# Kernel tuning notes

Measured on AMD Instinct MI355X. Metric: run time of the kernel, lower is better.

The kernel has to match this reference:

```python
import jax, jax.numpy as jnp
import numpy as np

OBS_DIM = 512
BACKBONE_DIMS = [1024, 1024, 512]
EXPERT_HIDDEN = 256
NUM_EXPERTS = 16
NUM_ACTIONS = 32
BATCH = 65536


def _glorot(key, shape):
    fan_in = shape[-2] if len(shape) >= 2 else shape[-1]
    return jax.random.normal(key, shape, dtype=jnp.float32) * (1.0 / np.sqrt(fan_in))


def setup_inputs() -> dict:
    key = jax.random.key(0)
    ks = jax.random.split(key, 16)
    inp = {}
    inp['obs'] = jax.random.normal(ks[0], (BATCH, OBS_DIM), dtype=jnp.float32)
    # shared backbone: 512->1024->1024->512 (Linear+ReLU+Dropout(eval=identity))
    dims = [OBS_DIM] + BACKBONE_DIMS
    for i in range(3):
        inp[f'Wb{i}'] = _glorot(ks[1 + i], (dims[i], dims[i + 1]))
        inp[f'bb{i}'] = jnp.zeros((dims[i + 1],), dtype=jnp.float32)
    # experts, batched over expert dim: 512->256->ReLU->256->32
    inp['We1'] = _glorot(ks[4], (NUM_EXPERTS, BACKBONE_DIMS[-1], EXPERT_HIDDEN))
    inp['be1'] = jnp.zeros((NUM_EXPERTS, EXPERT_HIDDEN), dtype=jnp.float32)
    inp['We2'] = _glorot(ks[5], (NUM_EXPERTS, EXPERT_HIDDEN, NUM_ACTIONS))
    inp['be2'] = jnp.zeros((NUM_EXPERTS, NUM_ACTIONS), dtype=jnp.float32)
    # motion selector: 512->256->128->16 + softmax
    inp['Ws0'] = _glorot(ks[6], (OBS_DIM, 256))
    inp['bs0'] = jnp.zeros((256,), dtype=jnp.float32)
    inp['Ws1'] = _glorot(ks[7], (256, 128))
    inp['bs1'] = jnp.zeros((128,), dtype=jnp.float32)
    inp['Ws2'] = _glorot(ks[8], (128, NUM_EXPERTS))
    inp['bs2'] = jnp.zeros((NUM_EXPERTS,), dtype=jnp.float32)
    return inp


def reference(obs, Wb0, bb0, Wb1, bb1, Wb2, bb2, We1, be1, We2, be2,
              Ws0, bs0, Ws1, bs1, Ws2, bs2):
    # shared backbone (Dropout is identity in eval/inference)
    h = jax.nn.relu(obs @ Wb0 + bb0)
    h = jax.nn.relu(h @ Wb1 + bb1)
    h = jax.nn.relu(h @ Wb2 + bb2)  # [B, 512]
    # all experts on shared features, as one batched GEMM
    eh = jax.nn.relu(jnp.einsum('bd,edh->beh', h, We1) + be1)       # [B, E, 256]
    expert_actions = jnp.einsum('beh,eha->bea', eh, We2) + be2       # [B, E, A]
    # motion selector (softmax fusion weights)
    s = jax.nn.relu(obs @ Ws0 + bs0)
    s = jax.nn.relu(s @ Ws1 + bs1)
    w = jax.nn.softmax(s @ Ws2 + bs2, axis=-1)                        # [B, E]
    # softmax-weighted fusion over experts
    fused = jnp.einsum('bea,be->ba', expert_actions, w)              # [B, A]
    return fused
```

## Files before the change

### kernel.cpp

```cpp
#include <hip/hip_runtime.h>
#include <hip/hip_bf16.h>
#include <stdint.h>

typedef __attribute__((ext_vector_type(8))) short short8;
typedef __attribute__((ext_vector_type(4))) float f32x4;

__device__ __forceinline__ float b2f(short s) {
    union { unsigned u; float f; } v; v.u = ((unsigned)(unsigned short)s) << 16; return v.f;
}
__device__ __forceinline__ short f2b(float f) {
    union { float f; unsigned u; } v; v.f = f;
    unsigned r = (v.u + 0x7FFF + ((v.u >> 16) & 1)) >> 16;
    return (short)r;
}

__device__ __forceinline__ void gload16(const void* g, void* l) {
    __builtin_amdgcn_global_load_lds(
        (const __attribute__((address_space(1))) void*)(uintptr_t)g,
        (__attribute__((address_space(3))) void*)(uintptr_t)l,
        16, 0, 0);
}

#define BAR()    asm volatile("s_barrier" ::: "memory")
#define WAITV0() asm volatile("s_waitcnt vmcnt(0)" ::: "memory")
#define WAITL0() asm volatile("s_waitcnt lgkmcnt(0)" ::: "memory")
#define SGB()    __builtin_amdgcn_sched_barrier(0)

__global__ __launch_bounds__(256) void cast_bf16_kernel(
    const float* __restrict__ src, short* __restrict__ dst, int n8) {
    int i = blockIdx.x * 256 + threadIdx.x;
    if (i >= n8) return;
    const float4* s = (const float4*)src + (size_t)i * 2;
    float4 x0 = s[0], x1 = s[1];
    short8 o;
    o[0] = f2b(x0.x); o[1] = f2b(x0.y); o[2] = f2b(x0.z); o[3] = f2b(x0.w);
    o[4] = f2b(x1.x); o[5] = f2b(x1.y); o[6] = f2b(x1.z); o[7] = f2b(x1.w);
    *((short8*)dst + i) = o;
}

__global__ __launch_bounds__(256) void transpose_cast_kernel(
    const float* __restrict__ W, short* __restrict__ Wt, int K, int N, int total) {
    int t = blockIdx.x * 256 + threadIdx.x;
    if (t >= total) return;
    const float* src = W + (size_t)blockIdx.y * K * N;
    short* dst = Wt + (size_t)blockIdx.y * K * N;
    int n = t % N;
    int k0 = (t / N) * 8;
    short8 o;
#pragma unroll
    for (int i = 0; i < 8; i++) o[i] = f2b(src[(size_t)(k0 + i) * N + n]);
    *(short8*)(dst + (size_t)n * K + k0) = o;
}

__global__ __launch_bounds__(256) void repack_We2_kernel(
    const float* __restrict__ We2, short* __restrict__ Bt2) {
    int t = blockIdx.x * 256 + threadIdx.x;
    int h0 = (t & 31) * 8;
    int a = (t >> 5) & 31;
    int e = t >> 10;
    short8 o;
#pragma unroll
    for (int j = 0; j < 8; j++) o[j] = f2b(We2[((size_t)e * 256 + h0 + j) * 32 + a]);
    *(short8*)(Bt2 + (size_t)a * 4096 + e * 256 + h0) = o;
}

__global__ __launch_bounds__(256, 3)
void gemm_bt_bias_relu(const short* __restrict__ A, const short* __restrict__ Bt,
                       const float* __restrict__ bias, short* __restrict__ C,
                       int M, int N, int K) {
    __shared__ __align__(16) short As[128 * 32];
    __shared__ __align__(16) short Bs[128 * 32];
    const int tid = threadIdx.x;
    const int w = tid >> 6, lane = tid & 63;
    const int tm = blockIdx.y * 128, tn = blockIdx.x * 128;
    const int wm = (w & 1) * 64, wn = (w >> 1) * 64;
    const int r = lane & 15, q = lane >> 4, qk = q * 8;

    const int c0 = w * 2, c1 = w * 2 + 1;
    const int srow0 = c0 * 16 + (lane >> 2);
    const int srow1 = c1 * 16 + (lane >> 2);
    const int skk = (lane & 3) * 8;
    const short* gA0 = A + (size_t)(tm + srow0) * K + skk;
    const short* gA1 = A + (size_t)(tm + srow1) * K + skk;
    const short* gB0 = Bt + (size_t)(tn + srow0) * K + skk;
    const short* gB1 = Bt + (size_t)(tn + srow1) * K + skk;
    short* lA0 = &As[c0 * 512]; short* lA1 = &As[c1 * 512];
    short* lB0 = &Bs[c0 * 512]; short* lB1 = &Bs[c1 * 512];

    f32x4 acc[4][4] = {};
    for (int k0 = 0; k0 < K; k0 += 32) {
        gload16(gA0 + k0, lA0);
        gload16(gA1 + k0, lA1);
        gload16(gB0 + k0, lB0);
        gload16(gB1 + k0, lB1);
        __syncthreads();
        short8 a[4], b[4];
#pragma unroll
        for (int i = 0; i < 4; i++) a[i] = *(const short8*)&As[(wm + i * 16 + r) * 32 + qk];
#pragma unroll
        for (int j = 0; j < 4; j++) b[j] = *(const short8*)&Bs[(wn + j * 16 + r) * 32 + qk];
#pragma unroll
        for (int i = 0; i < 4; i++)
#pragma unroll
            for (int j = 0; j < 4; j++)
                acc[i][j] = __builtin_amdgcn_mfma_f32_16x16x32_bf16(a[i], b[j], acc[i][j], 0, 0, 0);
        __syncthreads();
    }
#pragma unroll
    for (int j = 0; j < 4; j++) {
        int col = tn + wn + j * 16 + r;
        float bj = bias[col];
#pragma unroll
        for (int i = 0; i < 4; i++)
#pragma unroll
            for (int rr = 0; rr < 4; rr++) {
                int row = tm + wm + i * 16 + q * 4 + rr;
                float v = fmaxf(acc[i][j][rr] + bj, 0.f);
                C[(size_t)row * N + col] = f2b(v);
            }
    }
}

__global__ __launch_bounds__(256)
void selector_softmax(const short* __restrict__ s1, const short* __restrict__ Ws2t,
                      const float* __restrict__ bs2, float* __restrict__ wsel) {
    int tid = threadIdx.x;
    int row = blockIdx.x * 16 + (tid >> 4);
    int e = tid & 15;
    const short8* a = (const short8*)(s1 + (size_t)row * 128);
    const short8* b = (const short8*)(Ws2t + (size_t)e * 128);
    float acc = bs2[e];
#pragma unroll
    for (int kk = 0; kk < 16; ++kk) {
        short8 av = a[kk], bv = b[kk];
#pragma unroll
        for (int i = 0; i < 8; i++) acc = fmaf(b2f(av[i]), b2f(bv[i]), acc);
    }
    float m = acc;
#pragma unroll
    for (int off = 8; off >= 1; off >>= 1) m = fmaxf(m, __shfl_xor(m, off, 16));
    float ex = __expf(acc - m);
    float s = ex;
#pragma unroll
    for (int off = 8; off >= 1; off >>= 1) s += __shfl_xor(s, off, 16);
    wsel[(size_t)row * 16 + e] = ex / s;
}

template<int MODE>
__global__ __launch_bounds__(512, 2)
void gemm256(const short* __restrict__ A, const short* __restrict__ Bt,
             const float* __restrict__ bias, const float* __restrict__ wselp,
             short* __restrict__ C, int M, int N, int K) {
    extern __shared__ __align__(16) short lds[];
    const int tid = threadIdx.x;
    const int w = tid >> 6, lane = tid & 63;
    const int wr = w >> 2, wc = w & 3;

    const int gx = gridDim.x;
    const int b = blockIdx.y * gx + blockIdx.x;
    const int per = (gx * gridDim.y) >> 3;
    const int sb = (b & 7) * per + (b >> 3);
    const int bx = sb % gx, by = sb / gx;
    const int tm = by * 256, tn = bx * 256;

    const int rih = w * 8 + (lane >> 3);
    const int colel = (((lane & 7) ^ (lane >> 3)) << 3);
    const short* pA = A + (size_t)(tm + rih) * K + colel;
    const short* pB = Bt + (size_t)(tn + rih) * K + colel;
    const size_t rK64 = (size_t)64 * K, rK128 = (size_t)128 * K;
    short* const ldsw = lds + w * 512;

#define STG_A(buf, h, t) do { \
        const short* s_ = pA + (size_t)(h) * rK128 + (size_t)(t) * 64; \
        short* d_ = ldsw + (buf) * 32768 + (h) * 8192; \
        gload16(s_, d_); \
        gload16(s_ + rK64, d_ + 4096); } while (0)
#define STG_B(buf, h, t) do { \
        const short* s_ = pB + (size_t)(h) * rK128 + (size_t)(t) * 64; \
        short* d_ = ldsw + (buf) * 32768 + 16384 + (h) * 8192; \
        gload16(s_, d_); \
        gload16(s_ + rK64, d_ + 4096); } while (0)

    const int rA = lane & 15, q = lane >> 4;
    const int csw0 = ((q << 4)) ^ ((lane & 7) << 4);
    const int csw1 = (64 + (q << 4)) ^ ((lane & 7) << 4);
    const char* const ldsB_ = (const char*)lds;
    const int aBase0 = wr * 16384 + rA * 128;
    const int bBase0 = 32768 + (wc >> 1) * 16384 + ((wc & 1) * 64 + rA) * 128;

    f32x4 acc[8][4] = {};
    short8 a[4][2], b0[2][2], b1[2][2];
    const int nt = K >> 6;

    STG_A(0, 0, 0); STG_A(0, 1, 0); STG_B(0, 0, 0); STG_B(0, 1, 0);
    WAITV0(); BAR();

    for (int t = 0; t < nt; ++t) {
        const int cur = t & 1, nxt = cur ^ 1;
        const char* pa = ldsB_ + cur * 65536 + aBase0;
        const char* pb = ldsB_ + cur * 65536 + bBase0;
#pragma unroll
        for (int m = 0; m < 4; m++) {
            a[m][0] = *(const short8*)(pa + m * 2048 + csw0);
            a[m][1] = *(const short8*)(pa + m * 2048 + csw1);
        }
#pragma unroll
        for (int n = 0; n < 2; n++) {
            b0[n][0] = *(const short8*)(pb + n * 2048 + csw0);
            b0[n][1] = *(const short8*)(pb + n * 2048 + csw1);
        }
        if (t + 1 < nt) {
            STG_A(nxt, 0, t + 1); STG_A(nxt, 1, t + 1);
            STG_B(nxt, 0, t + 1); STG_B(nxt, 1, t + 1);
        }
        WAITL0(); SGB();
        __builtin_amdgcn_s_setprio(1);
#pragma unroll
        for (int m = 0; m < 4; m++)
#pragma unroll
            for (int n = 0; n < 2; n++) {
                acc[m][n] = __builtin_amdgcn_mfma_f32_16x16x32_bf16(a[m][0], b0[n][0], acc[m][n], 0, 0, 0);
                acc[m][n] = __builtin_amdgcn_mfma_f32_16x16x32_bf16(a[m][1], b0[n][1], acc[m][n], 0, 0, 0);
            }
        __builtin_amdgcn_s_setprio(0);
#pragma unroll
        for (int n = 0; n < 2; n++) {
            b1[n][0] = *(const short8*)(pb + (2 + n) * 2048 + csw0);
            b1[n][1] = *(const short8*)(pb + (2 + n) * 2048 + csw1);
        }
        WAITL0(); SGB();
        __builtin_amdgcn_s_setprio(1);
#pragma unroll
        for (int m = 0; m < 4; m++)
#pragma unroll
            for (int n = 0; n < 2; n++) {
                acc[m][2 + n] = __builtin_amdgcn_mfma_f32_16x16x32_bf16(a[m][0], b1[n][0], acc[m][2 + n], 0, 0, 0);
                acc[m][2 + n] = __builtin_amdgcn_mfma_f32_16x16x32_bf16(a[m][1], b1[n][1], acc[m][2 + n], 0, 0, 0);
            }
        __builtin_amdgcn_s_setprio(0);
#pragma unroll
        for (int m = 0; m < 4; m++) {
            a[m][0] = *(const short8*)(pa + (4 + m) * 2048 + csw0);
            a[m][1] = *(const short8*)(pa + (4 + m) * 2048 + csw1);
        }
        WAITL0(); SGB();
        __builtin_amdgcn_s_setprio(1);
#pragma unroll
        for (int m = 0; m < 4; m++)
#pragma unroll
            for (int n = 0; n < 2; n++) {
                acc[4 + m][2 + n] = __builtin_amdgcn_mfma_f32_16x16x32_bf16(a[m][0], b1[n][0], acc[4 + m][2 + n], 0, 0, 0);
                acc[4 + m][2 + n] = __builtin_amdgcn_mfma_f32_16x16x32_bf16(a[m][1], b1[n][1], acc[4 + m][2 + n], 0, 0, 0);
            }
        __builtin_amdgcn_s_setprio(0);
        __builtin_amdgcn_s_setprio(1);
#pragma unroll
        for (int m = 0; m < 4; m++)
#pragma unroll
            for (int n = 0; n < 2; n++) {
                acc[4 + m][n] = __builtin_amdgcn_mfma_f32_16x16x32_bf16(a[m][0], b0[n][0], acc[4 + m][n], 0, 0, 0);
                acc[4 + m][n] = __builtin_amdgcn_mfma_f32_16x16x32_bf16(a[m][1], b0[n][1], acc[4 + m][n], 0, 0, 0);
            }
        __builtin_amdgcn_s_setprio(0);
        WAITV0();
        BAR();
    }
#undef STG_A
#undef STG_B

    float biasv[4];
#pragma unroll
    for (int n = 0; n < 4; n++) biasv[n] = bias[tn + wc * 64 + n * 16 + rA];
    const int q4 = q * 4;
#pragma unroll
    for (int m = 0; m < 8; m++)
#pragma unroll
        for (int rr = 0; rr < 4; rr++) {
            const int row = tm + wr * 128 + m * 16 + q4 + rr;
            float ws = 1.f;
            if (MODE == 1) ws = wselp[(size_t)row * 16 + (tn >> 8)];
#pragma unroll
            for (int n = 0; n < 4; n++) {
                const int col = tn + wc * 64 + n * 16 + rA;
                float v = fmaxf(acc[m][n][rr] + biasv[n], 0.f);
                if (MODE == 1) v *= ws;
                C[(size_t)row * N + col] = f2b(v);
            }
        }
}

__global__ __launch_bounds__(256)
void fuse_gemm(const short* __restrict__ Aeh, const short* __restrict__ Bt2,
               const float* __restrict__ wsel, const float* __restrict__ be2,
               float* __restrict__ out, int accflag) {
    __shared__ __align__(16) short sA[2][128 * 64];
    const int tid = threadIdx.x;
    const int w = tid >> 6, lane = tid & 63;
    const int tm = blockIdx.x * 128;
    const int rih = w * 8 + (lane >> 3);
    const int colel = (((lane & 7) ^ (lane >> 3)) << 3);
    const short* pA = Aeh + (size_t)(tm + rih) * 2048 + colel;
    const int rA = lane & 15;
    const int csw0 = (((lane >> 4) << 4)) ^ ((lane & 7) << 4);
    const int csw1 = (64 + ((lane >> 4) << 4)) ^ ((lane & 7) << 4);
    const short* pBg = Bt2 + (size_t)rA * 4096 + ((lane >> 4) << 3);

    f32x4 acc[2][2] = {};
#define STG_E(buf, t) do { \
        const short* s_ = pA + (size_t)(t) * 64; \
        short* d_ = &sA[buf][w * 512]; \
        gload16(s_, d_); \
        gload16(s_ + (size_t)32 * 2048, d_ + 2048); \
        gload16(s_ + (size_t)64 * 2048, d_ + 4096); \
        gload16(s_ + (size_t)96 * 2048, d_ + 6144); } while (0)

    const int NT = 32;
    STG_E(0, 0);
    WAITV0(); BAR();
    for (int t = 0; t < NT; ++t) {
        const int cur = t & 1;
        if (t + 1 < NT) STG_E(cur ^ 1, t + 1);
        const char* pa = (const char*)&sA[cur][0] + (w * 32 + rA) * 128;
        short8 av[2][2], bv[2][2];
#pragma unroll
        for (int m = 0; m < 2; m++) {
            av[m][0] = *(const short8*)(pa + m * 2048 + csw0);
            av[m][1] = *(const short8*)(pa + m * 2048 + csw1);
        }
#pragma unroll
        for (int n = 0; n < 2; n++) {
            bv[n][0] = *(const short8*)(pBg + (size_t)n * 16 * 4096 + t * 64);
            bv[n][1] = *(const short8*)(pBg + (size_t)n * 16 * 4096 + t * 64 + 32);
        }
#pragma unroll
        for (int m = 0; m < 2; m++)
#pragma unroll
            for (int n = 0; n < 2; n++) {
                acc[m][n] = __builtin_amdgcn_mfma_f32_16x16x32_bf16(av[m][0], bv[n][0], acc[m][n], 0, 0, 0);
                acc[m][n] = __builtin_amdgcn_mfma_f32_16x16x32_bf16(av[m][1], bv[n][1], acc[m][n], 0, 0, 0);
            }
        WAITL0(); WAITV0(); BAR();
    }
#undef STG_E

    float be2v0[16], be2v1[16];
    if (!accflag) {
#pragma unroll
        for (int e = 0; e < 16; e++) {
            be2v0[e] = be2[e * 32 + rA];
            be2v1[e] = be2[e * 32 + 16 + rA];
        }
    }
    const int q4 = (lane >> 4) * 4;
#pragma unroll
    for (int m = 0; m < 2; m++)
#pragma unroll
        for (int rr = 0; rr < 4; rr++) {
            const int row = tm + w * 32 + m * 16 + q4 + rr;
            float v0 = acc[m][0][rr], v1 = acc[m][1][rr];
            if (!accflag) {
#pragma unroll
                for (int e = 0; e < 16; e++) {
                    float wv = wsel[(size_t)row * 16 + e];
                    v0 = fmaf(wv, be2v0[e], v0);
                    v1 = fmaf(wv, be2v1[e], v1);
                }
                out[(size_t)row * 32 + rA] = v0;
                out[(size_t)row * 32 + 16 + rA] = v1;
            } else {
                out[(size_t)row * 32 + rA] += v0;
                out[(size_t)row * 32 + 16 + rA] += v1;
            }
        }
}

extern "C" void kernel_launch(void* const* d_in, const int* in_sizes, int n_in,
                              void* d_out, int out_size, void* d_ws, size_t ws_size,
                              hipStream_t stream) {
    const float* obs = (const float*)d_in[0];
    const float* Wb0 = (const float*)d_in[1]; const float* bb0 = (const float*)d_in[2];
    const float* Wb1 = (const float*)d_in[3]; const float* bb1 = (const float*)d_in[4];
    const float* Wb2 = (const float*)d_in[5]; const float* bb2 = (const float*)d_in[6];
    const float* We1 = (const float*)d_in[7]; const float* be1 = (const float*)d_in[8];
    const float* We2 = (const float*)d_in[9]; const float* be2 = (const float*)d_in[10];
    const float* Ws0 = (const float*)d_in[11]; const float* bs0 = (const float*)d_in[12];
    const float* Ws1 = (const float*)d_in[13]; const float* bs1 = (const float*)d_in[14];
    const float* Ws2 = (const float*)d_in[15]; const float* bs2 = (const float*)d_in[16];

    const int B = 65536;
    char* ws = (char*)d_ws;
    size_t off = 0;
    auto alloc = [&](size_t bytes) { void* p = ws + off; off += (bytes + 255) & ~(size_t)255; return p; };
    short* obs_bf = (short*)alloc((size_t)B * 512 * 2);
    short* h1     = (short*)alloc((size_t)B * 1024 * 2);
    short* h2     = (short*)alloc((size_t)B * 1024 * 2);
    short* hbuf   = (short*)alloc((size_t)B * 512 * 2);
    short* s0     = (short*)alloc((size_t)B * 256 * 2);
    short* s1     = (short*)alloc((size_t)B * 128 * 2);
    float* wsel   = (float*)alloc((size_t)B * 16 * 4);
    short* Wb0t   = (short*)alloc((size_t)512 * 1024 * 2);
    short* Wb1t   = (short*)alloc((size_t)1024 * 1024 * 2);
    short* Wb2t   = (short*)alloc((size_t)1024 * 512 * 2);
    short* We1t   = (short*)alloc((size_t)16 * 512 * 256 * 2);
    short* Ws0t   = (short*)alloc((size_t)512 * 256 * 2);
    short* Ws1t   = (short*)alloc((size_t)256 * 128 * 2);
    short* Ws2t   = (short*)alloc((size_t)128 * 16 * 2);
    short* Bt2    = (short*)alloc((size_t)32 * 4096 * 2);
    short* s_eh = h1;

    static int inited = 0;
    if (!inited) {
        hipFuncSetAttribute(reinterpret_cast<const void*>(gemm256<0>),
                            hipFuncAttributeMaxDynamicSharedMemorySize, 131072);
        hipFuncSetAttribute(reinterpret_cast<const void*>(gemm256<1>),
                            hipFuncAttributeMaxDynamicSharedMemorySize, 131072);
        inited = 1;
    }

    cast_bf16_kernel<<<(B * 512 / 8 + 255) / 256, 256, 0, stream>>>(obs, obs_bf, B * 512 / 8);
    transpose_cast_kernel<<<dim3((1024 * 512 / 8 + 255) / 256, 1), 256, 0, stream>>>(Wb0, Wb0t, 512, 1024, 1024 * 512 / 8);
    transpose_cast_kernel<<<dim3((1024 * 1024 / 8 + 255) / 256, 1), 256, 0, stream>>>(Wb1, Wb1t, 1024, 1024, 1024 * 1024 / 8);
    transpose_cast_kernel<<<dim3((512 * 1024 / 8 + 255) / 256, 1), 256, 0, stream>>>(Wb2, Wb2t, 1024, 512, 512 * 1024 / 8);
    transpose_cast_kernel<<<dim3((256 * 512 / 8 + 255) / 256, 16), 256, 0, stream>>>(We1, We1t, 512, 256, 256 * 512 / 8);
    transpose_cast_kernel<<<dim3((256 * 512 / 8 + 255) / 256, 1), 256, 0, stream>>>(Ws0, Ws0t, 512, 256, 256 * 512 / 8);
    transpose_cast_kernel<<<dim3((128 * 256 / 8 + 255) / 256, 1), 256, 0, stream>>>(Ws1, Ws1t, 256, 128, 128 * 256 / 8);
    transpose_cast_kernel<<<dim3((16 * 128 / 8 + 255) / 256, 1), 256, 0, stream>>>(Ws2, Ws2t, 128, 16, 16 * 128 / 8);
    repack_We2_kernel<<<64, 256, 0, stream>>>(We2, Bt2);

    gemm256<0><<<dim3(1, B / 256), 512, 131072, stream>>>(obs_bf, Ws0t, bs0, nullptr, s0, B, 256, 512);
    gemm_bt_bias_relu<<<dim3(1, B / 128), 256, 0, stream>>>(s0, Ws1t, bs1, s1, B, 128, 256);
    selector_softmax<<<B / 16, 256, 0, stream>>>(s1, Ws2t, bs2, wsel);

    gemm256<0><<<dim3(4, B / 256), 512, 131072, stream>>>(obs_bf, Wb0t, bb0, nullptr, h1, B, 1024, 512);
    gemm256<0><<<dim3(4, B / 256), 512, 131072, stream>>>(h1, Wb1t, bb1, nullptr, h2, B, 1024, 1024);
    gemm256<0><<<dim3(2, B / 256), 512, 131072, stream>>>(h2, Wb2t, bb2, nullptr, hbuf, B, 512, 1024);

    for (int g = 0; g < 2; ++g) {
        gemm256<1><<<dim3(8, B / 256), 512, 131072, stream>>>(
            hbuf, We1t + (size_t)g * 8 * 256 * 512, be1 + g * 2048, wsel + g * 8,
            s_eh, B, 2048, 512);
        fuse_gemm<<<B / 128, 256, 0, stream>>>(
            s_eh, Bt2 + g * 2048, wsel, be2, (float*)d_out, g);
    }
}
```

Baseline: 1.117 ms.

## Fuse expert second-layer GEMM into expert first-layer epilogue with partial reduction

The second expert GEMM is now computed inside the epilogue of the expert first-layer kernel. Each 256-row tile's weighted hidden activations are staged in LDS and multiplied by that expert's We2 slice, and per-expert partial outputs are written as fp32. A small reduce kernel sums the 16 expert partials into an output pre-initialised with the weighted be2 bias. This removes the round trip of the large bf16 expert-hidden tensor through global memory and the separate fuse_gemm passes. The cost is a fp32 partial buffer (B*16*32 floats), an extra reduce pass, and B operands read straight from global memory in the epilogue.

```diff
diff --git a/kernel.cpp b/kernel.cpp
--- a/kernel.cpp
+++ b/kernel.cpp
@@ -50,18 +50,6 @@
 #pragma unroll
     for (int i = 0; i < 8; i++) o[i] = f2b(src[(size_t)(k0 + i) * N + n]);
     *(short8*)(dst + (size_t)n * K + k0) = o;
-}
-
-__global__ __launch_bounds__(256) void repack_We2_kernel(
-    const float* __restrict__ We2, short* __restrict__ Bt2) {
-    int t = blockIdx.x * 256 + threadIdx.x;
-    int h0 = (t & 31) * 8;
-    int a = (t >> 5) & 31;
-    int e = t >> 10;
-    short8 o;
-#pragma unroll
-    for (int j = 0; j < 8; j++) o[j] = f2b(We2[((size_t)e * 256 + h0 + j) * 32 + a]);
-    *(short8*)(Bt2 + (size_t)a * 4096 + e * 256 + h0) = o;
 }
 
 __global__ __launch_bounds__(256, 3)
@@ -146,11 +134,36 @@
     wsel[(size_t)row * 16 + e] = ex / s;
 }
 
+__global__ __launch_bounds__(256)
+void out_init_kernel(const float* __restrict__ wsel, const float* __restrict__ be2,
+                     float* __restrict__ out) {
+    int i = blockIdx.x * 256 + threadIdx.x;
+    int row = i >> 5, a = i & 31;
+    const float* wr = wsel + (size_t)row * 16;
+    float acc = 0.f;
+#pragma unroll
+    for (int e = 0; e < 16; e++) acc = fmaf(wr[e], be2[e * 32 + a], acc);
+    out[i] = acc;
+}
+
+__global__ __launch_bounds__(256)
+void reduce_kernel(const float* __restrict__ partial, float* __restrict__ out) {
+    int t = blockIdx.x * 256 + threadIdx.x;
+    int a4 = t & 7, i = t >> 3;
+    int by = i >> 8, r = i & 255;
+    const float* p = partial + (size_t)by * 16 * 8192 + r * 32 + a4 * 4;
+    f32x4 s = *(const f32x4*)(out + (size_t)i * 32 + a4 * 4);
+#pragma unroll
+    for (int bx = 0; bx < 16; bx++) s += *(const f32x4*)(p + (size_t)bx * 8192);
+    *(f32x4*)(out + (size_t)i * 32 + a4 * 4) = s;
+}
+
 template<int MODE>
 __global__ __launch_bounds__(512, 2)
 void gemm256(const short* __restrict__ A, const short* __restrict__ Bt,
              const float* __restrict__ bias, const float* __restrict__ wselp,
-             short* __restrict__ C, int M, int N, int K) {
+             const short* __restrict__ W2, short* __restrict__ C,
+             float* __restrict__ pout, int M, int N, int K) {
     extern __shared__ __align__(16) short lds[];
     const int tid = threadIdx.x;
     const int w = tid >> 6, lane = tid & 63;
@@ -268,10 +281,59 @@
 #undef STG_A
 #undef STG_B
 
+    const int q4 = q * 4;
     float biasv[4];
 #pragma unroll
     for (int n = 0; n < 4; n++) biasv[n] = bias[tn + wc * 64 + n * 16 + rA];
-    const int q4 = q * 4;
+
+    if (MODE == 2) {
+        const int e = tn >> 8;
+        char* ldsc = (char*)lds;
+#pragma unroll
+        for (int m = 0; m < 8; m++)
+#pragma unroll
+            for (int rr = 0; rr < 4; rr++) {
+                const int row = wr * 128 + m * 16 + q4 + rr;
+                const float ws = wselp[(size_t)(tm + row) * 16 + e];
+#pragma unroll
+                for (int n = 0; n < 4; n++) {
+                    const int col = wc * 64 + n * 16 + rA;
+                    const float v = fmaxf(acc[m][n][rr] + biasv[n], 0.f) * ws;
+                    *(short*)(ldsc + row * 512 + ((col * 2) ^ ((row & 7) << 4))) = f2b(v);
+                }
+            }
+        WAITL0(); BAR();
+        f32x4 g2[2][2] = {};
+#pragma unroll
+        for (int k2 = 0; k2 < 8; ++k2) {
+            short8 a2[2], b2[2];
+#pragma unroll
+            for (int m2 = 0; m2 < 2; m2++) {
+                const int row = w * 32 + m2 * 16 + rA;
+                a2[m2] = *(const short8*)(ldsc + row * 512 + ((k2 * 64 + q * 16) ^ ((row & 7) << 4)));
+            }
+#pragma unroll
+            for (int n2 = 0; n2 < 2; n2++)
+                b2[n2] = *(const short8*)(W2 + (size_t)(e * 32 + n2 * 16 + rA) * 256 + k2 * 32 + q * 8);
+#pragma unroll
+            for (int m2 = 0; m2 < 2; m2++)
+#pragma unroll
+                for (int n2 = 0; n2 < 2; n2++)
+                    g2[m2][n2] = __builtin_amdgcn_mfma_f32_16x16x32_bf16(a2[m2], b2[n2], g2[m2][n2], 0, 0, 0);
+        }
+        float* pp = pout + ((size_t)(tm >> 8) * 16 + e) * 8192;
+#pragma unroll
+        for (int m2 = 0; m2 < 2; m2++)
+#pragma unroll
+            for (int rr = 0; rr < 4; rr++) {
+                const int row = w * 32 + m2 * 16 + q4 + rr;
+#pragma unroll
+                for (int n2 = 0; n2 < 2; n2++)
+                    pp[row * 32 + n2 * 16 + rA] = g2[m2][n2][rr];
+            }
+        return;
+    }
+
 #pragma unroll
     for (int m = 0; m < 8; m++)
 #pragma unroll
@@ -285,91 +347,6 @@
                 float v = fmaxf(acc[m][n][rr] + biasv[n], 0.f);
                 if (MODE == 1) v *= ws;
                 C[(size_t)row * N + col] = f2b(v);
-            }
-        }
-}
-
-__global__ __launch_bounds__(256)
-void fuse_gemm(const short* __restrict__ Aeh, const short* __restrict__ Bt2,
-               const float* __restrict__ wsel, const float* __restrict__ be2,
-               float* __restrict__ out, int accflag) {
-    __shared__ __align__(16) short sA[2][128 * 64];
-    const int tid = threadIdx.x;
-    const int w = tid >> 6, lane = tid & 63;
-    const int tm = blockIdx.x * 128;
-    const int rih = w * 8 + (lane >> 3);
-    const int colel = (((lane & 7) ^ (lane >> 3)) << 3);
-    const short* pA = Aeh + (size_t)(tm + rih) * 2048 + colel;
-    const int rA = lane & 15;
-    const int csw0 = (((lane >> 4) << 4)) ^ ((lane & 7) << 4);
-    const int csw1 = (64 + ((lane >> 4) << 4)) ^ ((lane & 7) << 4);
-    const short* pBg = Bt2 + (size_t)rA * 4096 + ((lane >> 4) << 3);
-
-    f32x4 acc[2][2] = {};
-#define STG_E(buf, t) do { \
-        const short* s_ = pA + (size_t)(t) * 64; \
-        short* d_ = &sA[buf][w * 512]; \
-        gload16(s_, d_); \
-        gload16(s_ + (size_t)32 * 2048, d_ + 2048); \
-        gload16(s_ + (size_t)64 * 2048, d_ + 4096); \
-        gload16(s_ + (size_t)96 * 2048, d_ + 6144); } while (0)
-
-    const int NT = 32;
-    STG_E(0, 0);
-    WAITV0(); BAR();
-    for (int t = 0; t < NT; ++t) {
-        const int cur = t & 1;
-        if (t + 1 < NT) STG_E(cur ^ 1, t + 1);
-        const char* pa = (const char*)&sA[cur][0] + (w * 32 + rA) * 128;
-        short8 av[2][2], bv[2][2];
-#pragma unroll
-        for (int m = 0; m < 2; m++) {
-            av[m][0] = *(const short8*)(pa + m * 2048 + csw0);
-            av[m][1] = *(const short8*)(pa + m * 2048 + csw1);
-        }
-#pragma unroll
-        for (int n = 0; n < 2; n++) {
-            bv[n][0] = *(const short8*)(pBg + (size_t)n * 16 * 4096 + t * 64);
-            bv[n][1] = *(const short8*)(pBg + (size_t)n * 16 * 4096 + t * 64 + 32);
-        }
-#pragma unroll
-        for (int m = 0; m < 2; m++)
-#pragma unroll
-            for (int n = 0; n < 2; n++) {
-                acc[m][n] = __builtin_amdgcn_mfma_f32_16x16x32_bf16(av[m][0], bv[n][0], acc[m][n], 0, 0, 0);
-                acc[m][n] = __builtin_amdgcn_mfma_f32_16x16x32_bf16(av[m][1], bv[n][1], acc[m][n], 0, 0, 0);
-            }
-        WAITL0(); WAITV0(); BAR();
-    }
-#undef STG_E
-
-    float be2v0[16], be2v1[16];
-    if (!accflag) {
-#pragma unroll
-        for (int e = 0; e < 16; e++) {
-            be2v0[e] = be2[e * 32 + rA];
-            be2v1[e] = be2[e * 32 + 16 + rA];
-        }
-    }
-    const int q4 = (lane >> 4) * 4;
-#pragma unroll
-    for (int m = 0; m < 2; m++)
-#pragma unroll
-        for (int rr = 0; rr < 4; rr++) {
-            const int row = tm + w * 32 + m * 16 + q4 + rr;
-            float v0 = acc[m][0][rr], v1 = acc[m][1][rr];
-            if (!accflag) {
-#pragma unroll
-                for (int e = 0; e < 16; e++) {
-                    float wv = wsel[(size_t)row * 16 + e];
-                    v0 = fmaf(wv, be2v0[e], v0);
-                    v1 = fmaf(wv, be2v1[e], v1);
-                }
-                out[(size_t)row * 32 + rA] = v0;
-                out[(size_t)row * 32 + 16 + rA] = v1;
-            } else {
-                out[(size_t)row * 32 + rA] += v0;
-                out[(size_t)row * 32 + 16 + rA] += v1;
             }
         }
 }
@@ -402,17 +379,17 @@
     short* Wb1t   = (short*)alloc((size_t)1024 * 1024 * 2);
     short* Wb2t   = (short*)alloc((size_t)1024 * 512 * 2);
     short* We1t   = (short*)alloc((size_t)16 * 512 * 256 * 2);
+    short* We2t   = (short*)alloc((size_t)16 * 256 * 32 * 2);
     short* Ws0t   = (short*)alloc((size_t)512 * 256 * 2);
     short* Ws1t   = (short*)alloc((size_t)256 * 128 * 2);
     short* Ws2t   = (short*)alloc((size_t)128 * 16 * 2);
-    short* Bt2    = (short*)alloc((size_t)32 * 4096 * 2);
-    short* s_eh = h1;
+    float* partial = (float*)h1;
 
     static int inited = 0;
     if (!inited) {
         hipFuncSetAttribute(reinterpret_cast<const void*>(gemm256<0>),
                             hipFuncAttributeMaxDynamicSharedMemorySize, 131072);
-        hipFuncSetAttribute(reinterpret_cast<const void*>(gemm256<1>),
+        hipFuncSetAttribute(reinterpret_cast<const void*>(gemm256<2>),
                             hipFuncAttributeMaxDynamicSharedMemorySize, 131072);
         inited = 1;
     }
@@ -422,24 +399,21 @@
     transpose_cast_kernel<<<dim3((1024 * 1024 / 8 + 255) / 256, 1), 256, 0, stream>>>(Wb1, Wb1t, 1024, 1024, 1024 * 1024 / 8);
     transpose_cast_kernel<<<dim3((512 * 1024 / 8 + 255) / 256, 1), 256, 0, stream>>>(Wb2, Wb2t, 1024, 512, 512 * 1024 / 8);
     transpose_cast_kernel<<<dim3((256 * 512 / 8 + 255) / 256, 16), 256, 0, stream>>>(We1, We1t, 512, 256, 256 * 512 / 8);
+    transpose_cast_kernel<<<dim3((32 * 256 / 8 + 255) / 256, 16), 256, 0, stream>>>(We2, We2t, 256, 32, 32 * 256 / 8);
     transpose_cast_kernel<<<dim3((256 * 512 / 8 + 255) / 256, 1), 256, 0, stream>>>(Ws0, Ws0t, 512, 256, 256 * 512 / 8);
     transpose_cast_kernel<<<dim3((128 * 256 / 8 + 255) / 256, 1), 256, 0, stream>>>(Ws1, Ws1t, 256, 128, 128 * 256 / 8);
     transpose_cast_kernel<<<dim3((16 * 128 / 8 + 255) / 256, 1), 256, 0, stream>>>(Ws2, Ws2t, 128, 16, 16 * 128 / 8);
-    repack_We2_kernel<<<64, 256, 0, stream>>>(We2, Bt2);
-
-    gemm256<0><<<dim3(1, B / 256), 512, 131072, stream>>>(obs_bf, Ws0t, bs0, nullptr, s0, B, 256, 512);
+
+    gemm256<0><<<dim3(1, B / 256), 512, 131072, stream>>>(obs_bf, Ws0t, bs0, nullptr, nullptr, s0, nullptr, B, 256, 512);
     gemm_bt_bias_relu<<<dim3(1, B / 128), 256, 0, stream>>>(s0, Ws1t, bs1, s1, B, 128, 256);
     selector_softmax<<<B / 16, 256, 0, stream>>>(s1, Ws2t, bs2, wsel);
-
-    gemm256<0><<<dim3(4, B / 256), 512, 131072, stream>>>(obs_bf, Wb0t, bb0, nullptr, h1, B, 1024, 512);
-    gemm256<0><<<dim3(4, B / 256), 512, 131072, stream>>>(h1, Wb1t, bb1, nullptr, h2, B, 1024, 1024);
-    gemm256<0><<<dim3(2, B / 256), 512, 131072, stream>>>(h2, Wb2t, bb2, nullptr, hbuf, B, 512, 1024);
-
-    for (int g = 0; g < 2; ++g) {
-        gemm256<1><<<dim3(8, B / 256), 512, 131072, stream>>>(
-            hbuf, We1t + (size_t)g * 8 * 256 * 512, be1 + g * 2048, wsel + g * 8,
-            s_eh, B, 2048, 512);
-        fuse_gemm<<<B / 128, 256, 0, stream>>>(
-            s_eh, Bt2 + g * 2048, wsel, be2, (float*)d_out, g);
-    }
-}
+    out_init_kernel<<<B * 32 / 256, 256, 0, stream>>>(wsel, be2, (float*)d_out);
+
+    gemm256<0><<<dim3(4, B / 256), 512, 131072, stream>>>(obs_bf, Wb0t, bb0, nullptr, nullptr, h1, nullptr, B, 1024, 512);
+    gemm256<0><<<dim3(4, B / 256), 512, 131072, stream>>>(h1, Wb1t, bb1, nullptr, nullptr, h2, nullptr, B, 1024, 1024);
+    gemm256<0><<<dim3(2, B / 256), 512, 131072, stream>>>(h2, Wb2t, bb2, nullptr, nullptr, hbuf, nullptr, B, 512, 1024);
+
+    gemm256<2><<<dim3(16, B / 256), 512, 131072, stream>>>(
+        hbuf, We1t, be1, wsel, We2t, nullptr, partial, B, 4096, 512);
+    reduce_kernel<<<B * 8 / 256, 256, 0, stream>>>(partial, (float*)d_out);
+}
```

New measurement: 1.033 ms. 1.08x faster.
